# Optimization experiments

Measured on AMD Instinct MI355X. Metric: run time of the kernel, lower is better.

## Reference

```python
import jax, jax.numpy as jnp
import numpy as np

N, B, I = 64, 32, 1
EMBED, ACT, DETER, STOCH, HIDDEN = 1536, 16, 2048, 512, 1024
EPS = 1e-5


def _ln(x, g, b):
    m = jnp.mean(x, -1, keepdims=True)
    v = jnp.mean((x - m) ** 2, -1, keepdims=True)
    return (x - m) / jnp.sqrt(v + EPS) * g + b


def setup_inputs() -> dict:
    key = jax.random.key(0)
    ks = jax.random.split(key, 24)
    s = 0.02
    d = {
        "embed": jax.random.normal(ks[0], (N, B, EMBED), jnp.float32),
        "action": jax.random.normal(ks[1], (N, B, ACT), jnp.float32),
        "reset": jnp.zeros((N, B), jnp.bool_),
        "h0": jnp.zeros((B * I, DETER), jnp.float32),
        "z0": jnp.zeros((B * I, STOCH), jnp.float32),
        "noises": jax.random.normal(ks[2], (N, B, I, STOCH), jnp.float32),
        # params
        "W_z": jax.random.normal(ks[3], (HIDDEN, STOCH)) * s,
        "b_z": jnp.zeros((HIDDEN,)),
        "W_a": jax.random.normal(ks[4], (HIDDEN, ACT)) * s,
        "ln_in_g": jnp.ones((HIDDEN,)), "ln_in_b": jnp.zeros((HIDDEN,)),
        "gru_Wih": jax.random.normal(ks[5], (3 * DETER, HIDDEN)) * s,
        "gru_Whh": jax.random.normal(ks[6], (3 * DETER, DETER)) * s,
        "gru_bih": jnp.zeros((3 * DETER,)), "gru_bhh": jnp.zeros((3 * DETER,)),
        "W_ph": jax.random.normal(ks[7], (HIDDEN, DETER)) * s,
        "b_ph": jnp.zeros((HIDDEN,)),
        "W_pe": jax.random.normal(ks[8], (HIDDEN, EMBED)) * s,
        "ln_post_g": jnp.ones((HIDDEN,)), "ln_post_b": jnp.zeros((HIDDEN,)),
        "W_post": jax.random.normal(ks[9], (2 * STOCH, HIDDEN)) * s,
        "b_post": jnp.zeros((2 * STOCH,)),
        "W_prh": jax.random.normal(ks[10], (HIDDEN, DETER)) * s,
        "b_prh": jnp.zeros((HIDDEN,)),
        "ln_pr_g": jnp.ones((HIDDEN,)), "ln_pr_b": jnp.zeros((HIDDEN,)),
        "W_pr": jax.random.normal(ks[11], (2 * STOCH, HIDDEN)) * s,
        "b_pr": jnp.zeros((2 * STOCH,)),
    }
    return d


def _core(embed, action, reset, h0, z0, noises,
          W_z, b_z, W_a, ln_in_g, ln_in_b,
          gru_Wih, gru_Whh, gru_bih, gru_bhh,
          W_ph, b_ph, W_pe, ln_post_g, ln_post_b, W_post, b_post,
          W_prh, b_prh, ln_pr_g, ln_pr_b, W_pr, b_pr):
    n, b = embed.shape[:2]
    # expand to (n, b*I, .) ; I == 1
    embeds = embed.reshape(n, b * I, -1)
    actions = action.reshape(n, b * I, -1)
    masks = (~reset).astype(jnp.float32).reshape(n, b * I, 1)
    noise = noises.reshape(n, b * I, -1)

    def step(carry, xs):
        h, z = carry
        e_t, a_t, m_t, n_t = xs
        h = h * m_t
        z = z * m_t
        x = z @ W_z.T + b_z + a_t @ W_a.T
        za = jax.nn.elu(_ln(x, ln_in_g, ln_in_b))
        # torch GRUCell
        gi = za @ gru_Wih.T + gru_bih
        gh = h @ gru_Whh.T + gru_bhh
        gi_r, gi_u, gi_n = jnp.split(gi, 3, -1)
        gh_r, gh_u, gh_n = jnp.split(gh, 3, -1)
        r = jax.nn.sigmoid(gi_r + gh_r)
        u = jax.nn.sigmoid(gi_u + gh_u)
        cand = jnp.tanh(gi_n + r * gh_n)
        h_new = (1.0 - u) * cand + u * h
        x = h_new @ W_ph.T + b_ph + e_t @ W_pe.T
        post_in = jax.nn.elu(_ln(x, ln_post_g, ln_post_b))
        post = post_in @ W_post.T + b_post
        mean, std_raw = jnp.split(post, 2, -1)
        std = jax.nn.softplus(std_raw) + 0.1
        sample = mean + std * n_t
        return (h_new, sample), (post, h_new, sample)

    (h_last, z_last), (posts, states_h, samples) = jax.lax.scan(
        step, (h0, z0), (embeds, actions, masks, noise))

    # batch prior over all h
    x = states_h @ W_prh.T + b_prh
    x = jax.nn.elu(_ln(x, ln_pr_g, ln_pr_b))
    priors = x @ W_pr.T + b_pr
    features = jnp.concatenate([states_h, samples], -1)

    rs = lambda t: t.reshape(n, b, I, -1)
    return rs(priors), rs(posts), rs(samples), rs(features), h_last, z_last


def reference(embed, action, reset, h0, z0, noises,
              W_z, b_z, W_a, ln_in_g, ln_in_b,
              gru_Wih, gru_Whh, gru_bih, gru_bhh,
              W_ph, b_ph, W_pe, ln_post_g, ln_post_b, W_post, b_post,
              W_prh, b_prh, ln_pr_g, ln_pr_b, W_pr, b_pr):
    return _core(embed, action, reset, h0, z0, noises,
                 W_z, b_z, W_a, ln_in_g, ln_in_b,
                 gru_Wih, gru_Whh, gru_bih, gru_bhh,
                 W_ph, b_ph, W_pe, ln_post_g, ln_post_b, W_post, b_post,
                 W_prh, b_prh, ln_pr_g, ln_pr_b, W_pr, b_pr)
```

## Files before the change

### kernel.cpp

```cpp
#include <hip/hip_runtime.h>
#include <hip/hip_bf16.h>
#include <stdint.h>

#define NSTEP 64
#define BATCH 32
#define EMBED_D 1536
#define ACT_D 16
#define DETER 2048
#define STOCH 512
#define HIDDEN 1024
#define FEAT 2560
#define NBLK 256

typedef __attribute__((ext_vector_type(8))) short bf16x8;
typedef __attribute__((ext_vector_type(4))) float f32x4;

#define MFMA16 __builtin_amdgcn_mfma_f32_16x16x32_bf16
#define AGENT __HIP_MEMORY_SCOPE_AGENT

__device__ __forceinline__ float eluf(float x) { return x > 0.f ? x : expf(x) - 1.f; }
__device__ __forceinline__ float sigf(float x) { return 1.f / (1.f + expf(-x)); }
__device__ __forceinline__ unsigned short f2bf(float f) {
    __hip_bfloat16 h = __float2bfloat16(f);
    return __builtin_bit_cast(unsigned short, h);
}
__device__ __forceinline__ float bf2f(unsigned short u) {
    unsigned v = ((unsigned)u) << 16;
    return __builtin_bit_cast(float, v);
}

__device__ __forceinline__ void stc_u32(unsigned* p, unsigned v) {
    __hip_atomic_store(p, v, __ATOMIC_RELAXED, AGENT);
}
__device__ __forceinline__ void stc_u64(unsigned long long* p, unsigned long long v) {
    __hip_atomic_store(p, v, __ATOMIC_RELAXED, AGENT);
}
__device__ __forceinline__ unsigned long long ldc_u64(const unsigned long long* p) {
    return __hip_atomic_load(p, __ATOMIC_RELAXED, AGENT);
}
__device__ __forceinline__ float ldc_f32(const float* p) {
    return __hip_atomic_load(p, __ATOMIC_RELAXED, AGENT);
}
__device__ __forceinline__ int ldc_i32(const int* p) {
    return __hip_atomic_load(p, __ATOMIC_RELAXED, AGENT);
}
__device__ __forceinline__ void stc_i32(int* p, int v) {
    __hip_atomic_store(p, v, __ATOMIC_RELAXED, AGENT);
}
__device__ __forceinline__ bf16x8 ldc_bf8(const unsigned short* p) {
    union { unsigned long long q[2]; bf16x8 v; } u;
    u.q[0] = ldc_u64((const unsigned long long*)p);
    u.q[1] = ldc_u64((const unsigned long long*)(p + 4));
    return u.v;
}
__device__ __forceinline__ ushort4 ldc_us4(const unsigned short* p) {
    unsigned long long q = ldc_u64((const unsigned long long*)p);
    return __builtin_bit_cast(ushort4, q);
}

__device__ __forceinline__ void gbar3(int* flags, int* release, int epoch) {
    asm volatile("s_waitcnt vmcnt(0)" ::: "memory");
    __syncthreads();
    if (blockIdx.x == 0) {
        int tid = threadIdx.x;
        if (tid >= 1 && tid < NBLK) {
            while (ldc_i32(&flags[tid * 32]) < epoch) __builtin_amdgcn_s_sleep(4);
        }
        asm volatile("" ::: "memory");
        __syncthreads();
        if (tid < 32) stc_i32(&release[tid * 32], epoch);
    } else {
        if (threadIdx.x == 0) {
            stc_i32(&flags[blockIdx.x * 32], epoch);
            int* rel = &release[(blockIdx.x & 31) * 32];
            while (ldc_i32(rel) < epoch) __builtin_amdgcn_s_sleep(4);
        }
        asm volatile("" ::: "memory");
        __syncthreads();
    }
}

__global__ __launch_bounds__(256) void k_cvt_all(
    const float* __restrict__ s0, unsigned short* __restrict__ d0,
    const float* __restrict__ s1, unsigned short* __restrict__ d1,
    const float* __restrict__ s2, unsigned short* __restrict__ d2,
    const float* __restrict__ s3, unsigned short* __restrict__ d3,
    const float* __restrict__ s4, unsigned short* __restrict__ d4)
{
    long long e = ((long long)blockIdx.x * 256 + threadIdx.x) * 4;
    const float* src; unsigned short* dst; long long off;
    if (e < 524288)        { src = s0; dst = d0; off = e; }
    else if (e < 6815744)  { src = s1; dst = d1; off = e - 524288; }
    else if (e < 19398656) { src = s2; dst = d2; off = e - 6815744; }
    else if (e < 21495808) { src = s3; dst = d3; off = e - 19398656; }
    else if (e < 22544384) { src = s4; dst = d4; off = e - 21495808; }
    else return;
    float4 v = *reinterpret_cast<const float4*>(src + off);
    ushort4 o;
    o.x = f2bf(v.x); o.y = f2bf(v.y); o.z = f2bf(v.z); o.w = f2bf(v.w);
    *reinterpret_cast<ushort4*>(dst + off) = o;
}

__global__ __launch_bounds__(256) void k_setup(
    const float* __restrict__ h0, const float* __restrict__ z0,
    const uint8_t* __restrict__ reset0,
    float* __restrict__ h0m, unsigned short* __restrict__ h16m0,
    unsigned short* __restrict__ z16m, int* __restrict__ flags)
{
    int gid = blockIdx.x * 256 + threadIdx.x;
    int idx = gid * 4;
    if (idx < BATCH * DETER) {
        int b = idx >> 11;
        float m = reset0[b] ? 0.f : 1.f;
        float4 v = *reinterpret_cast<const float4*>(h0 + idx);
        v.x *= m; v.y *= m; v.z *= m; v.w *= m;
        *reinterpret_cast<float4*>(h0m + idx) = v;
        ushort4 o;
        o.x = f2bf(v.x); o.y = f2bf(v.y); o.z = f2bf(v.z); o.w = f2bf(v.w);
        *reinterpret_cast<ushort4*>(h16m0 + idx) = o;
    } else if (idx < BATCH * DETER + BATCH * STOCH) {
        int zi = idx - BATCH * DETER;
        int b = zi >> 9;
        float m = reset0[b] ? 0.f : 1.f;
        float4 v = *reinterpret_cast<const float4*>(z0 + zi);
        ushort4 o;
        o.x = f2bf(v.x * m); o.y = f2bf(v.y * m); o.z = f2bf(v.z * m); o.w = f2bf(v.w * m);
        *reinterpret_cast<ushort4*>(z16m + zi) = o;
    }
    if (gid < 9216) flags[gid] = 0;
}

__global__ __launch_bounds__(256) void k_preA(
    const float* __restrict__ action, const float* __restrict__ Wa,
    const float* __restrict__ bz, float* __restrict__ preA)
{
    __shared__ float al[16];
    int r = blockIdx.x, t = threadIdx.x;
    if (t < 16) al[t] = action[r * 16 + t];
    __syncthreads();
#pragma unroll
    for (int c = 0; c < 4; ++c) {
        int j = t + c * 256;
        const float* wr = Wa + j * 16;
        float s = bz[j];
#pragma unroll
        for (int k = 0; k < 16; ++k) s += al[k] * wr[k];
        preA[(size_t)r * 1024 + j] = s;
    }
}

__global__ __launch_bounds__(256) void gemm_mfma(
    const float* __restrict__ A, int lda,
    const float* __restrict__ B, int ldb,
    const float* __restrict__ bias,
    float* __restrict__ C, int ldc, int K)
{
    __shared__ unsigned short Alds[64 * 72];
    __shared__ unsigned short Blds[64 * 72];
    int t = threadIdx.x;
    int nb = blockIdx.x, mb = blockIdx.y;
    int w = t >> 6, l = t & 63, l15 = l & 15, kg = l >> 4;
    f32x4 acc[4] = {{0,0,0,0},{0,0,0,0},{0,0,0,0},{0,0,0,0}};
    int srow = t >> 2, skq = (t & 3) * 16;
    const float* Asrc = A + (size_t)(mb * 64 + srow) * lda + skq;
    const float* Bsrc = B + (size_t)(nb * 64 + srow) * ldb + skq;
    unsigned short* Adst = &Alds[srow * 72 + skq];
    unsigned short* Bdst = &Blds[srow * 72 + skq];
    for (int kt = 0; kt < K; kt += 64) {
        __syncthreads();
#pragma unroll
        for (int c = 0; c < 16; c += 4) {
            float4 va = *reinterpret_cast<const float4*>(Asrc + kt + c);
            float4 vb = *reinterpret_cast<const float4*>(Bsrc + kt + c);
            ushort4 oa, ob;
            oa.x = f2bf(va.x); oa.y = f2bf(va.y); oa.z = f2bf(va.z); oa.w = f2bf(va.w);
            ob.x = f2bf(vb.x); ob.y = f2bf(vb.y); ob.z = f2bf(vb.z); ob.w = f2bf(vb.w);
            *reinterpret_cast<ushort4*>(Adst + c) = oa;
            *reinterpret_cast<ushort4*>(Bdst + c) = ob;
        }
        __syncthreads();
#pragma unroll
        for (int ks = 0; ks < 2; ks++) {
            bf16x8 a = *reinterpret_cast<const bf16x8*>(&Alds[(w * 16 + l15) * 72 + ks * 32 + kg * 8]);
#pragma unroll
            for (int nt = 0; nt < 4; nt++) {
                bf16x8 b = *reinterpret_cast<const bf16x8*>(&Blds[(nt * 16 + l15) * 72 + ks * 32 + kg * 8]);
                acc[nt] = MFMA16(a, b, acc[nt], 0, 0, 0);
            }
        }
    }
#pragma unroll
    for (int nt = 0; nt < 4; nt++) {
        int n = nb * 64 + nt * 16 + l15;
        float bv = bias[n];
#pragma unroll
        for (int i = 0; i < 4; i++) {
            C[(size_t)(mb * 64 + w * 16 + kg * 4 + i) * ldc + n] = acc[nt][i] + bv;
        }
    }
}

__global__ __launch_bounds__(256) void ln_elu_rows(
    float* __restrict__ X, const float* __restrict__ g, const float* __restrict__ bb)
{
    __shared__ float sbuf[256], qbuf[256];
    int r = blockIdx.x, t = threadIdx.x;
    float* row = X + (size_t)r * HIDDEN;
    float4 v = reinterpret_cast<const float4*>(row)[t];
    sbuf[t] = (v.x + v.y) + (v.z + v.w);
    qbuf[t] = (v.x * v.x + v.y * v.y) + (v.z * v.z + v.w * v.w);
    __syncthreads();
    for (int off = 128; off > 0; off >>= 1) {
        if (t < off) { sbuf[t] += sbuf[t + off]; qbuf[t] += qbuf[t + off]; }
        __syncthreads();
    }
    float mean = sbuf[0] / HIDDEN;
    float var = qbuf[0] / HIDDEN - mean * mean;
    float rstd = rsqrtf(var + 1e-5f);
    float4 gg = reinterpret_cast<const float4*>(g)[t];
    float4 bv = reinterpret_cast<const float4*>(bb)[t];
    float4 o;
    o.x = eluf((v.x - mean) * rstd * gg.x + bv.x);
    o.y = eluf((v.y - mean) * rstd * gg.y + bv.y);
    o.z = eluf((v.z - mean) * rstd * gg.z + bv.z);
    o.w = eluf((v.w - mean) * rstd * gg.w + bv.w);
    reinterpret_cast<float4*>(row)[t] = o;
}

__global__ __launch_bounds__(256) void k_copy_last(
    const float* __restrict__ feat63, const float* __restrict__ samp63,
    float* __restrict__ hlast, float* __restrict__ zlast)
{
    int i = blockIdx.x * 256 + threadIdx.x;
    if (i < BATCH * DETER) {
        int b = i / DETER, k = i % DETER;
        hlast[i] = feat63[(size_t)b * FEAT + k];
    }
    if (i < BATCH * STOCH) zlast[i] = samp63[i];
}

struct ScanArgs {
    const unsigned short *Wz16, *Wih16, *Whh16, *Wph16, *Wpo16;
    const float *bih, *bhh, *b_post;
    const float *ln_in_g, *ln_in_b, *ln_post_g, *ln_post_b;
    const float *h0m;
    const uint8_t *reset;
    const float *noises;
    float *postsPreA;
    float *priorsPreE;
    float *samples;
    float *feats;
    unsigned short *z16m, *x1b, *x2b, *h16u, *h16m0, *h16m1;
    float *x1parts, *x2parts;
    int *flags, *release;
};

__device__ __forceinline__ void ln_stats(const float* __restrict__ parts, float* stat, int tid) {
    if (tid < 32) {
        float s = 0.f, q = 0.f;
        for (int i = 0; i < 64; ++i) {
            union { unsigned long long u; float f[2]; } c;
            c.u = ldc_u64((const unsigned long long*)(parts + (size_t)(i * 32 + tid) * 2));
            s += c.f[0]; q += c.f[1];
        }
        float mean = s * (1.f / 1024.f);
        float var = q * (1.f / 1024.f) - mean * mean;
        stat[tid] = mean;
        stat[32 + tid] = rsqrtf(var + 1e-5f);
    }
}

__device__ __forceinline__ void ln_fill(unsigned short* Asm, const unsigned short* __restrict__ src,
                                        const float* __restrict__ g, const float* __restrict__ bb,
                                        const float* stat, int tid) {
    int row = tid & 31, kb = (tid >> 5) * 128;
    float mean = stat[row], rstd = stat[32 + row];
#pragma unroll 4
    for (int c = 0; c < 16; ++c) {
        int k = kb + c * 8;
        ushort4 u0 = ldc_us4(src + (size_t)row * 1024 + k);
        ushort4 u1 = ldc_us4(src + (size_t)row * 1024 + k + 4);
        float4 g0 = *reinterpret_cast<const float4*>(g + k);
        float4 g1 = *reinterpret_cast<const float4*>(g + k + 4);
        float4 b0 = *reinterpret_cast<const float4*>(bb + k);
        float4 b1 = *reinterpret_cast<const float4*>(bb + k + 4);
        ushort4 o0, o1;
        o0.x = f2bf(eluf((bf2f(u0.x) - mean) * rstd * g0.x + b0.x));
        o0.y = f2bf(eluf((bf2f(u0.y) - mean) * rstd * g0.y + b0.y));
        o0.z = f2bf(eluf((bf2f(u0.z) - mean) * rstd * g0.z + b0.z));
        o0.w = f2bf(eluf((bf2f(u0.w) - mean) * rstd * g0.w + b0.w));
        o1.x = f2bf(eluf((bf2f(u1.x) - mean) * rstd * g1.x + b1.x));
        o1.y = f2bf(eluf((bf2f(u1.y) - mean) * rstd * g1.y + b1.y));
        o1.z = f2bf(eluf((bf2f(u1.z) - mean) * rstd * g1.z + b1.z));
        o1.w = f2bf(eluf((bf2f(u1.w) - mean) * rstd * g1.w + b1.w));
        *reinterpret_cast<ushort4*>(Asm + row * 1032 + k) = o0;
        *reinterpret_cast<ushort4*>(Asm + row * 1032 + k + 4) = o1;
    }
}

__global__ __launch_bounds__(256, 1) void k_scan(ScanArgs a) {
    __shared__ char smem[90112];
    unsigned short* Asm = (unsigned short*)smem;
    float* cbuf = (float*)(smem + 66048);
    float* stat = (float*)(smem + 66048 + 8192);

    const int bid = blockIdx.x;
    const int tid = threadIdx.x;
    const int w = tid >> 6, l = tid & 63, l15 = l & 15, kg = l >> 4;
    int epoch = 0;

    for (int t = 0; t < NSTEP; ++t) {
        const float* preA_t = a.postsPreA + (size_t)t * 32768;
        const float* preE_t = a.priorsPreE + (size_t)t * 32768;
        float* posts_t = a.postsPreA + (size_t)t * 32768;
        float* samples_t = a.samples + (size_t)t * 16384;
        float* feats_t = a.feats + (size_t)t * 81920;
        const float* featsPrev = a.feats + (size_t)(t - 1) * 81920;
        const unsigned short* h16cur = (t & 1) ? a.h16m1 : a.h16m0;
        unsigned short* h16nxt = (t & 1) ? a.h16m0 : a.h16m1;

        if (bid < 64) {
            int j0 = bid * 16;
            const unsigned short* A0 = a.z16m + l15 * 512 + w * 128 + kg * 8;
            const unsigned short* A1 = A0 + 16 * 512;
            const unsigned short* Bp = a.Wz16 + (size_t)(j0 + l15) * 512 + w * 128 + kg * 8;
            f32x4 c0 = {0,0,0,0}, c1 = {0,0,0,0};
#pragma unroll
            for (int ks = 0; ks < 4; ++ks) {
                bf16x8 b = *reinterpret_cast<const bf16x8*>(Bp + ks * 32);
                c0 = MFMA16(ldc_bf8(A0 + ks * 32), b, c0, 0, 0, 0);
                c1 = MFMA16(ldc_bf8(A1 + ks * 32), b, c1, 0, 0, 0);
            }
#pragma unroll
            for (int i = 0; i < 4; ++i) {
                cbuf[w * 512 + (kg * 4 + i) * 16 + l15] = c0[i];
                cbuf[w * 512 + (16 + kg * 4 + i) * 16 + l15] = c1[i];
            }
            __syncthreads();
            int r = tid >> 3, c2 = (tid & 7) * 2;
            int base = r * 16 + c2;
            float v0 = cbuf[base] + cbuf[512 + base] + cbuf[1024 + base] + cbuf[1536 + base]
                     + preA_t[r * 1024 + j0 + c2];
            float v1 = cbuf[base + 1] + cbuf[512 + base + 1] + cbuf[1024 + base + 1] + cbuf[1536 + base + 1]
                     + preA_t[r * 1024 + j0 + c2 + 1];
            unsigned short u0 = f2bf(v0), u1 = f2bf(v1);
            stc_u32((unsigned*)(a.x1b + (size_t)r * 1024 + j0 + c2),
                    (unsigned)u0 | ((unsigned)u1 << 16));
            float w0 = bf2f(u0), w1 = bf2f(u1);
            float s = w0 + w1, q = w0 * w0 + w1 * w1;
            s += __shfl_xor(s, 1); q += __shfl_xor(q, 1);
            s += __shfl_xor(s, 2); q += __shfl_xor(q, 2);
            s += __shfl_xor(s, 4); q += __shfl_xor(q, 4);
            if ((tid & 7) == 0) {
                union { float f[2]; unsigned long long u; } pu;
                pu.f[0] = s; pu.f[1] = q;
                stc_u64((unsigned long long*)(a.x1parts + ((size_t)bid * 32 + r) * 2), pu.u);
            }
        }
        epoch++; gbar3(a.flags, a.release, epoch);

        if (bid < 128) {
            int j0 = bid * 16;
            ln_stats(a.x1parts, stat, tid);
            __syncthreads();
            ln_fill(Asm, a.x1b, a.ln_in_g, a.ln_in_b, stat, tid);
            __syncthreads();
            bool isI = (w < 2);
            int mt = w & 1;
            f32x4 cr = {0,0,0,0}, cu = {0,0,0,0}, cn = {0,0,0,0};
            if (isI) {
                const unsigned short* ap = Asm + (mt * 16 + l15) * 1032 + kg * 8;
                const unsigned short* br = a.Wih16 + (size_t)(j0 + l15) * 1024 + kg * 8;
                const unsigned short* bu = br + (size_t)2048 * 1024;
                const unsigned short* bn = bu + (size_t)2048 * 1024;
#pragma unroll 8
                for (int ks = 0; ks < 32; ++ks) {
                    bf16x8 av = *reinterpret_cast<const bf16x8*>(ap + ks * 32);
                    cr = MFMA16(av, *reinterpret_cast<const bf16x8*>(br + ks * 32), cr, 0, 0, 0);
                    cu = MFMA16(av, *reinterpret_cast<const bf16x8*>(bu + ks * 32), cu, 0, 0, 0);
                    cn = MFMA16(av, *reinterpret_cast<const bf16x8*>(bn + ks * 32), cn, 0, 0, 0);
                }
            } else {
                const unsigned short* ap = h16cur + (size_t)(mt * 16 + l15) * 2048 + kg * 8;
                const unsigned short* br = a.Whh16 + (size_t)(j0 + l15) * 2048 + kg * 8;
                const unsigned short* bu = br + (size_t)2048 * 2048;
                const unsigned short* bn = bu + (size_t)2048 * 2048;
#pragma unroll 8
                for (int ks = 0; ks < 64; ++ks) {
                    bf16x8 av = ldc_bf8(ap + ks * 32);
                    cr = MFMA16(av, *reinterpret_cast<const bf16x8*>(br + ks * 32), cr, 0, 0, 0);
                    cu = MFMA16(av, *reinterpret_cast<const bf16x8*>(bu + ks * 32), cu, 0, 0, 0);
                    cn = MFMA16(av, *reinterpret_cast<const bf16x8*>(bn + ks * 32), cn, 0, 0, 0);
                }
#pragma unroll
                for (int i = 0; i < 4; ++i) {
                    cbuf[((mt * 3 + 0) * 16 + kg * 4 + i) * 16 + l15] = cr[i];
                    cbuf[((mt * 3 + 1) * 16 + kg * 4 + i) * 16 + l15] = cu[i];
                    cbuf[((mt * 3 + 2) * 16 + kg * 4 + i) * 16 + l15] = cn[i];
                }
            }
            __syncthreads();
            if (isI) {
                int j = j0 + l15;
                float bihr = a.bih[j], bihu = a.bih[j + 2048], bihn = a.bih[j + 4096];
                float bhhr = a.bhh[j], bhhu = a.bhh[j + 2048], bhhn = a.bhh[j + 4096];
#pragma unroll
                for (int i = 0; i < 4; ++i) {
                    int b = mt * 16 + kg * 4 + i;
                    float gr = cr[i] + bihr, gu = cu[i] + bihu, gn = cn[i] + bihn;
                    float hr = cbuf[((mt * 3 + 0) * 16 + kg * 4 + i) * 16 + l15] + bhhr;
                    float hu = cbuf[((mt * 3 + 1) * 16 + kg * 4 + i) * 16 + l15] + bhhu;
                    float hn = cbuf[((mt * 3 + 2) * 16 + kg * 4 + i) * 16 + l15] + bhhn;
                    float r = sigf(gr + hr), u = sigf(gu + hu);
                    float cand = tanhf(gn + r * hn);
                    float m = a.reset[t * 32 + b] ? 0.f : 1.f;
                    float hpv = (t == 0) ? a.h0m[b * 2048 + j]
                                         : ldc_f32(featsPrev + (size_t)b * 2560 + j);
                    float hnew = (1.f - u) * cand + u * (m * hpv);
                    cbuf[1536 + b * 16 + l15] = hnew;
                }
            }
            __syncthreads();
            {
                int b = tid >> 3, c2 = (tid & 7) * 2;
                float h0v = cbuf[1536 + b * 16 + c2], h1v = cbuf[1536 + b * 16 + c2 + 1];
                int j = j0 + c2;
                union { float f[2]; unsigned long long u; } fu;
                fu.f[0] = h0v; fu.f[1] = h1v;
                stc_u64((unsigned long long*)(feats_t + (size_t)b * 2560 + j), fu.u);
                unsigned short g0 = f2bf(h0v), g1 = f2bf(h1v);
                stc_u32((unsigned*)(a.h16u + (size_t)b * 2048 + j),
                        (unsigned)g0 | ((unsigned)g1 << 16));
                float mn = (t < 63) ? (a.reset[(t + 1) * 32 + b] ? 0.f : 1.f) : 1.f;
                unsigned short n0 = f2bf(h0v * mn), n1 = f2bf(h1v * mn);
                stc_u32((unsigned*)(h16nxt + (size_t)b * 2048 + j),
                        (unsigned)n0 | ((unsigned)n1 << 16));
            }
        }
        epoch++; gbar3(a.flags, a.release, epoch);

        if (bid < 64) {
            int j0 = bid * 16;
            const unsigned short* A0 = a.h16u + l15 * 2048 + w * 512 + kg * 8;
            const unsigned short* A1 = A0 + 16 * 2048;
            const unsigned short* Bp = a.Wph16 + (size_t)(j0 + l15) * 2048 + w * 512 + kg * 8;
            f32x4 c0 = {0,0,0,0}, c1 = {0,0,0,0};
#pragma unroll 8
            for (int ks = 0; ks < 16; ++ks) {
                bf16x8 b = *reinterpret_cast<const bf16x8*>(Bp + ks * 32);
                c0 = MFMA16(ldc_bf8(A0 + ks * 32), b, c0, 0, 0, 0);
                c1 = MFMA16(ldc_bf8(A1 + ks * 32), b, c1, 0, 0, 0);
            }
#pragma unroll
            for (int i = 0; i < 4; ++i) {
                cbuf[w * 512 + (kg * 4 + i) * 16 + l15] = c0[i];
                cbuf[w * 512 + (16 + kg * 4 + i) * 16 + l15] = c1[i];
            }
            __syncthreads();
            int r = tid >> 3, c2 = (tid & 7) * 2;
            int base = r * 16 + c2;
            float v0 = cbuf[base] + cbuf[512 + base] + cbuf[1024 + base] + cbuf[1536 + base]
                     + preE_t[r * 1024 + j0 + c2];
            float v1 = cbuf[base + 1] + cbuf[512 + base + 1] + cbuf[1024 + base + 1] + cbuf[1536 + base + 1]
                     + preE_t[r * 1024 + j0 + c2 + 1];
            unsigned short u0 = f2bf(v0), u1 = f2bf(v1);
            stc_u32((unsigned*)(a.x2b + (size_t)r * 1024 + j0 + c2),
                    (unsigned)u0 | ((unsigned)u1 << 16));
            float w0 = bf2f(u0), w1 = bf2f(u1);
            float s = w0 + w1, q = w0 * w0 + w1 * w1;
            s += __shfl_xor(s, 1); q += __shfl_xor(q, 1);
            s += __shfl_xor(s, 2); q += __shfl_xor(q, 2);
            s += __shfl_xor(s, 4); q += __shfl_xor(q, 4);
            if ((tid & 7) == 0) {
                union { float f[2]; unsigned long long u; } pu;
                pu.f[0] = s; pu.f[1] = q;
                stc_u64((unsigned long long*)(a.x2parts + ((size_t)bid * 32 + r) * 2), pu.u);
            }
        }
        epoch++; gbar3(a.flags, a.release, epoch);

        if (bid < 32) {
            int j0 = bid * 16;
            ln_stats(a.x2parts, stat, tid);
            __syncthreads();
            ln_fill(Asm, a.x2b, a.ln_post_g, a.ln_post_b, stat, tid);
            __syncthreads();
            int tile = w >> 1, mt = w & 1;
            const unsigned short* ap = Asm + (mt * 16 + l15) * 1032 + kg * 8;
            int n = (tile == 0) ? (j0 + l15) : (512 + j0 + l15);
            const unsigned short* Bp = a.Wpo16 + (size_t)n * 1024 + kg * 8;
            f32x4 c = {0,0,0,0};
#pragma unroll 8
            for (int ks = 0; ks < 32; ++ks) {
                c = MFMA16(*reinterpret_cast<const bf16x8*>(ap + ks * 32),
                           *reinterpret_cast<const bf16x8*>(Bp + ks * 32), c, 0, 0, 0);
            }
#pragma unroll
            for (int i = 0; i < 4; ++i)
                cbuf[(tile * 2 + mt) * 256 + (kg * 4 + i) * 16 + l15] = c[i];
            __syncthreads();
            int b = tid >> 3, c2 = (tid & 7) * 2;
            int j = j0 + c2;
            int ib = (b >> 4) * 256 + (b & 15) * 16;
            float pm0 = cbuf[ib + c2] + a.b_post[j];
            float pm1 = cbuf[ib + c2 + 1] + a.b_post[j + 1];
            float ps0 = cbuf[512 + ib + c2] + a.b_post[512 + j];
            float ps1 = cbuf[512 + ib + c2 + 1] + a.b_post[512 + j + 1];
            posts_t[(size_t)b * 1024 + j] = pm0;
            posts_t[(size_t)b * 1024 + j + 1] = pm1;
            posts_t[(size_t)b * 1024 + 512 + j] = ps0;
            posts_t[(size_t)b * 1024 + 512 + j + 1] = ps1;
            float sp0 = fmaxf(ps0, 0.f) + log1pf(expf(-fabsf(ps0)));
            float sp1 = fmaxf(ps1, 0.f) + log1pf(expf(-fabsf(ps1)));
            float n0v = a.noises[(size_t)t * 16384 + b * 512 + j];
            float n1v = a.noises[(size_t)t * 16384 + b * 512 + j + 1];
            float smp0 = pm0 + (sp0 + 0.1f) * n0v;
            float smp1 = pm1 + (sp1 + 0.1f) * n1v;
            samples_t[(size_t)b * 512 + j] = smp0;
            samples_t[(size_t)b * 512 + j + 1] = smp1;
            feats_t[(size_t)b * 2560 + 2048 + j] = smp0;
            feats_t[(size_t)b * 2560 + 2048 + j + 1] = smp1;
            float mn = (t < 63) ? (a.reset[(t + 1) * 32 + b] ? 0.f : 1.f) : 1.f;
            unsigned short z0_ = f2bf(smp0 * mn), z1_ = f2bf(smp1 * mn);
            stc_u32((unsigned*)(a.z16m + (size_t)b * 512 + j),
                    (unsigned)z0_ | ((unsigned)z1_ << 16));
        }
        epoch++; gbar3(a.flags, a.release, epoch);
    }
}

#define WS_WZ16   ((size_t)0)
#define WS_WIH16  ((size_t)1048576)
#define WS_WHH16  ((size_t)13631488)
#define WS_WPH16  ((size_t)38797312)
#define WS_WPO16  ((size_t)42991616)
#define WS_Z16M   ((size_t)45088768)
#define WS_H16M0  ((size_t)45121536)
#define WS_H16M1  ((size_t)45252608)
#define WS_H16U   ((size_t)45383680)
#define WS_H0M    ((size_t)45514752)
#define WS_X1B    ((size_t)45776896)
#define WS_X2B    ((size_t)45842432)
#define WS_X1P    ((size_t)45907968)
#define WS_X2P    ((size_t)45924352)
#define WS_FLAGS  ((size_t)45940736)
#define WS_REL    ((size_t)45973504)
#define WS_PRX    WS_WIH16

extern "C" void kernel_launch(void* const* d_in, const int* in_sizes, int n_in,
                              void* d_out, int out_size, void* d_ws, size_t ws_size,
                              hipStream_t stream)
{
    (void)in_sizes; (void)n_in; (void)out_size; (void)ws_size;
    const float*   embed  = (const float*)d_in[0];
    const float*   action = (const float*)d_in[1];
    const uint8_t* reset  = (const uint8_t*)d_in[2];
    const float*   h0     = (const float*)d_in[3];
    const float*   z0     = (const float*)d_in[4];
    const float*   noises = (const float*)d_in[5];
    const float*   W_z    = (const float*)d_in[6];
    const float*   b_z    = (const float*)d_in[7];
    const float*   W_a    = (const float*)d_in[8];
    const float*   ln_in_g = (const float*)d_in[9];
    const float*   ln_in_b = (const float*)d_in[10];
    const float*   Wih    = (const float*)d_in[11];
    const float*   Whh    = (const float*)d_in[12];
    const float*   bih    = (const float*)d_in[13];
    const float*   bhh    = (const float*)d_in[14];
    const float*   W_ph   = (const float*)d_in[15];
    const float*   b_ph   = (const float*)d_in[16];
    const float*   W_pe   = (const float*)d_in[17];
    const float*   ln_post_g = (const float*)d_in[18];
    const float*   ln_post_b = (const float*)d_in[19];
    const float*   W_post = (const float*)d_in[20];
    const float*   b_post = (const float*)d_in[21];
    const float*   W_prh  = (const float*)d_in[22];
    const float*   b_prh  = (const float*)d_in[23];
    const float*   ln_pr_g = (const float*)d_in[24];
    const float*   ln_pr_b = (const float*)d_in[25];
    const float*   W_pr   = (const float*)d_in[26];
    const float*   b_pr   = (const float*)d_in[27];

    float* out     = (float*)d_out;
    float* priors  = out;
    float* posts   = out + 2097152;
    float* samples = out + 4194304;
    float* feats   = out + 5242880;
    float* hlast   = out + 10485760;
    float* zlast   = out + 10551296;

    char* ws = (char*)d_ws;
    unsigned short* Wz16  = (unsigned short*)(ws + WS_WZ16);
    unsigned short* Wih16 = (unsigned short*)(ws + WS_WIH16);
    unsigned short* Whh16 = (unsigned short*)(ws + WS_WHH16);
    unsigned short* Wph16 = (unsigned short*)(ws + WS_WPH16);
    unsigned short* Wpo16 = (unsigned short*)(ws + WS_WPO16);
    unsigned short* z16m  = (unsigned short*)(ws + WS_Z16M);
    unsigned short* h16m0 = (unsigned short*)(ws + WS_H16M0);
    unsigned short* h16m1 = (unsigned short*)(ws + WS_H16M1);
    unsigned short* h16u  = (unsigned short*)(ws + WS_H16U);
    float*          h0m   = (float*)(ws + WS_H0M);
    unsigned short* x1b   = (unsigned short*)(ws + WS_X1B);
    unsigned short* x2b   = (unsigned short*)(ws + WS_X2B);
    float*          x1p   = (float*)(ws + WS_X1P);
    float*          x2p   = (float*)(ws + WS_X2P);
    int*            flags = (int*)(ws + WS_FLAGS);
    int*            release = (int*)(ws + WS_REL);
    float*          prx   = (float*)(ws + WS_PRX);

    dim3 blk(256);

    k_cvt_all<<<dim3(22016), blk, 0, stream>>>(W_z, Wz16, Wih, Wih16, Whh, Whh16,
                                               W_ph, Wph16, W_post, Wpo16);
    k_setup<<<dim3(80), blk, 0, stream>>>(h0, z0, reset, h0m, h16m0, z16m, flags);

    k_preA<<<dim3(2048), blk, 0, stream>>>(action, W_a, b_z, posts);
    gemm_mfma<<<dim3(16, 32), blk, 0, stream>>>(embed, EMBED_D, W_pe, EMBED_D, b_ph,
                                                priors, HIDDEN, EMBED_D);

    ScanArgs sa;
    sa.Wz16 = Wz16; sa.Wih16 = Wih16; sa.Whh16 = Whh16; sa.Wph16 = Wph16; sa.Wpo16 = Wpo16;
    sa.bih = bih; sa.bhh = bhh; sa.b_post = b_post;
    sa.ln_in_g = ln_in_g; sa.ln_in_b = ln_in_b; sa.ln_post_g = ln_post_g; sa.ln_post_b = ln_post_b;
    sa.h0m = h0m; sa.reset = reset; sa.noises = noises;
    sa.postsPreA = posts; sa.priorsPreE = priors; sa.samples = samples; sa.feats = feats;
    sa.z16m = z16m; sa.x1b = x1b; sa.x2b = x2b; sa.h16u = h16u;
    sa.h16m0 = h16m0; sa.h16m1 = h16m1;
    sa.x1parts = x1p; sa.x2parts = x2p;
    sa.flags = flags; sa.release = release;
    k_scan<<<dim3(NBLK), blk, 0, stream>>>(sa);

    gemm_mfma<<<dim3(16, 32), blk, 0, stream>>>(feats, FEAT, W_prh, DETER, b_prh,
                                                prx, HIDDEN, DETER);
    ln_elu_rows<<<dim3(2048), blk, 0, stream>>>(prx, ln_pr_g, ln_pr_b);
    gemm_mfma<<<dim3(16, 32), blk, 0, stream>>>(prx, HIDDEN, W_pr, HIDDEN, b_pr,
                                                priors, HIDDEN, HIDDEN);

    k_copy_last<<<dim3(256), blk, 0, stream>>>(
        feats + (size_t)(NSTEP - 1) * BATCH * FEAT,
        samples + (size_t)(NSTEP - 1) * BATCH * STOCH,
        hlast, zlast);
}
```

Measured before the change: 4.676 ms.

## Double scan block size and split GRU K-dimension across eight waves

The persistent scan kernel now launches with 512 threads per block. The GRU stage splits each input-side and hidden-side matmul's K dimension in half across twice as many waves, then reduces the partial sums through shared memory before the gate math. The aim is to shorten the per-step critical path, which is dominated by streaming the GRU weights. Other stages leave the extra waves idle behind tid<256 guards. This adds shared-memory reduction traffic and raises per-block register pressure.

```diff
diff --git a/kernel.cpp b/kernel.cpp
--- a/kernel.cpp
+++ b/kernel.cpp
@@ -246,10 +246,7 @@
     const float *h0m;
     const uint8_t *reset;
     const float *noises;
-    float *postsPreA;
-    float *priorsPreE;
-    float *samples;
-    float *feats;
+    float *postsPreA, *priorsPreE, *samples, *feats;
     unsigned short *z16m, *x1b, *x2b, *h16u, *h16m0, *h16m1;
     float *x1parts, *x2parts;
     int *flags, *release;
@@ -298,11 +295,13 @@
     }
 }
 
-__global__ __launch_bounds__(256, 1) void k_scan(ScanArgs a) {
-    __shared__ char smem[90112];
+__global__ __launch_bounds__(512, 1) void k_scan(ScanArgs a) {
+    __shared__ char smem[93184];
     unsigned short* Asm = (unsigned short*)smem;
-    float* cbuf = (float*)(smem + 66048);
-    float* stat = (float*)(smem + 66048 + 8192);
+    float* cbuf  = (float*)(smem + 66048);
+    float* stat  = (float*)(smem + 66048 + 8192);
+    float* stat2 = (float*)(smem + 90624);
+    float* hbuf  = (float*)(smem + 91136);
 
     const int bid = blockIdx.x;
     const int tid = threadIdx.x;
@@ -321,109 +320,112 @@
 
         if (bid < 64) {
             int j0 = bid * 16;
-            const unsigned short* A0 = a.z16m + l15 * 512 + w * 128 + kg * 8;
-            const unsigned short* A1 = A0 + 16 * 512;
-            const unsigned short* Bp = a.Wz16 + (size_t)(j0 + l15) * 512 + w * 128 + kg * 8;
-            f32x4 c0 = {0,0,0,0}, c1 = {0,0,0,0};
-#pragma unroll
-            for (int ks = 0; ks < 4; ++ks) {
-                bf16x8 b = *reinterpret_cast<const bf16x8*>(Bp + ks * 32);
-                c0 = MFMA16(ldc_bf8(A0 + ks * 32), b, c0, 0, 0, 0);
-                c1 = MFMA16(ldc_bf8(A1 + ks * 32), b, c1, 0, 0, 0);
-            }
-#pragma unroll
-            for (int i = 0; i < 4; ++i) {
-                cbuf[w * 512 + (kg * 4 + i) * 16 + l15] = c0[i];
-                cbuf[w * 512 + (16 + kg * 4 + i) * 16 + l15] = c1[i];
-            }
-            __syncthreads();
-            int r = tid >> 3, c2 = (tid & 7) * 2;
-            int base = r * 16 + c2;
-            float v0 = cbuf[base] + cbuf[512 + base] + cbuf[1024 + base] + cbuf[1536 + base]
-                     + preA_t[r * 1024 + j0 + c2];
-            float v1 = cbuf[base + 1] + cbuf[512 + base + 1] + cbuf[1024 + base + 1] + cbuf[1536 + base + 1]
-                     + preA_t[r * 1024 + j0 + c2 + 1];
-            unsigned short u0 = f2bf(v0), u1 = f2bf(v1);
-            stc_u32((unsigned*)(a.x1b + (size_t)r * 1024 + j0 + c2),
-                    (unsigned)u0 | ((unsigned)u1 << 16));
-            float w0 = bf2f(u0), w1 = bf2f(u1);
-            float s = w0 + w1, q = w0 * w0 + w1 * w1;
-            s += __shfl_xor(s, 1); q += __shfl_xor(q, 1);
-            s += __shfl_xor(s, 2); q += __shfl_xor(q, 2);
-            s += __shfl_xor(s, 4); q += __shfl_xor(q, 4);
-            if ((tid & 7) == 0) {
-                union { float f[2]; unsigned long long u; } pu;
-                pu.f[0] = s; pu.f[1] = q;
-                stc_u64((unsigned long long*)(a.x1parts + ((size_t)bid * 32 + r) * 2), pu.u);
+            if (tid < 256) {
+                const unsigned short* A0 = a.z16m + l15 * 512 + w * 128 + kg * 8;
+                const unsigned short* A1 = A0 + 16 * 512;
+                const unsigned short* Bp = a.Wz16 + (size_t)(j0 + l15) * 512 + w * 128 + kg * 8;
+                f32x4 c0 = {0,0,0,0}, c1 = {0,0,0,0};
+#pragma unroll
+                for (int ks = 0; ks < 4; ++ks) {
+                    bf16x8 b = *reinterpret_cast<const bf16x8*>(Bp + ks * 32);
+                    c0 = MFMA16(ldc_bf8(A0 + ks * 32), b, c0, 0, 0, 0);
+                    c1 = MFMA16(ldc_bf8(A1 + ks * 32), b, c1, 0, 0, 0);
+                }
+#pragma unroll
+                for (int i = 0; i < 4; ++i) {
+                    cbuf[w * 512 + (kg * 4 + i) * 16 + l15] = c0[i];
+                    cbuf[w * 512 + (16 + kg * 4 + i) * 16 + l15] = c1[i];
+                }
+            }
+            __syncthreads();
+            if (tid < 256) {
+                int r = tid >> 3, c2 = (tid & 7) * 2;
+                int base = r * 16 + c2;
+                float v0 = cbuf[base] + cbuf[512 + base] + cbuf[1024 + base] + cbuf[1536 + base]
+                         + preA_t[r * 1024 + j0 + c2];
+                float v1 = cbuf[base + 1] + cbuf[512 + base + 1] + cbuf[1024 + base + 1] + cbuf[1536 + base + 1]
+                         + preA_t[r * 1024 + j0 + c2 + 1];
+                unsigned short u0 = f2bf(v0), u1 = f2bf(v1);
+                stc_u32((unsigned*)(a.x1b + (size_t)r * 1024 + j0 + c2),
+                        (unsigned)u0 | ((unsigned)u1 << 16));
+                float w0 = bf2f(u0), w1 = bf2f(u1);
+                float s = w0 + w1, q = w0 * w0 + w1 * w1;
+                s += __shfl_xor(s, 1); q += __shfl_xor(q, 1);
+                s += __shfl_xor(s, 2); q += __shfl_xor(q, 2);
+                s += __shfl_xor(s, 4); q += __shfl_xor(q, 4);
+                if ((tid & 7) == 0) {
+                    union { float f[2]; unsigned long long u; } pu;
+                    pu.f[0] = s; pu.f[1] = q;
+                    stc_u64((unsigned long long*)(a.x1parts + ((size_t)bid * 32 + r) * 2), pu.u);
+                }
             }
         }
         epoch++; gbar3(a.flags, a.release, epoch);
 
         if (bid < 128) {
             int j0 = bid * 16;
-            ln_stats(a.x1parts, stat, tid);
-            __syncthreads();
-            ln_fill(Asm, a.x1b, a.ln_in_g, a.ln_in_b, stat, tid);
-            __syncthreads();
-            bool isI = (w < 2);
-            int mt = w & 1;
+            ln_stats(a.x1parts, stat2, tid);
+            __syncthreads();
+            if (tid < 256) ln_fill(Asm, a.x1b, a.ln_in_g, a.ln_in_b, stat2, tid);
+            __syncthreads();
             f32x4 cr = {0,0,0,0}, cu = {0,0,0,0}, cn = {0,0,0,0};
-            if (isI) {
-                const unsigned short* ap = Asm + (mt * 16 + l15) * 1032 + kg * 8;
-                const unsigned short* br = a.Wih16 + (size_t)(j0 + l15) * 1024 + kg * 8;
+            if (w < 4) {
+                int rowgrp = w & 1, kh = w >> 1;
+                const unsigned short* ap = Asm + (rowgrp * 16 + l15) * 1032 + kh * 512 + kg * 8;
+                const unsigned short* br = a.Wih16 + (size_t)(j0 + l15) * 1024 + kh * 512 + kg * 8;
                 const unsigned short* bu = br + (size_t)2048 * 1024;
                 const unsigned short* bn = bu + (size_t)2048 * 1024;
-#pragma unroll 8
-                for (int ks = 0; ks < 32; ++ks) {
+#pragma unroll 4
+                for (int ks = 0; ks < 16; ++ks) {
                     bf16x8 av = *reinterpret_cast<const bf16x8*>(ap + ks * 32);
                     cr = MFMA16(av, *reinterpret_cast<const bf16x8*>(br + ks * 32), cr, 0, 0, 0);
                     cu = MFMA16(av, *reinterpret_cast<const bf16x8*>(bu + ks * 32), cu, 0, 0, 0);
                     cn = MFMA16(av, *reinterpret_cast<const bf16x8*>(bn + ks * 32), cn, 0, 0, 0);
                 }
             } else {
-                const unsigned short* ap = h16cur + (size_t)(mt * 16 + l15) * 2048 + kg * 8;
-                const unsigned short* br = a.Whh16 + (size_t)(j0 + l15) * 2048 + kg * 8;
+                int idx = w - 4, rowgrp = idx & 1, kh = idx >> 1;
+                const unsigned short* hp = h16cur + (size_t)(rowgrp * 16 + l15) * 2048 + kh * 1024 + kg * 8;
+                const unsigned short* br = a.Whh16 + (size_t)(j0 + l15) * 2048 + kh * 1024 + kg * 8;
                 const unsigned short* bu = br + (size_t)2048 * 2048;
                 const unsigned short* bn = bu + (size_t)2048 * 2048;
-#pragma unroll 8
-                for (int ks = 0; ks < 64; ++ks) {
-                    bf16x8 av = ldc_bf8(ap + ks * 32);
+#pragma unroll 4
+                for (int ks = 0; ks < 32; ++ks) {
+                    bf16x8 av = ldc_bf8(hp + ks * 32);
                     cr = MFMA16(av, *reinterpret_cast<const bf16x8*>(br + ks * 32), cr, 0, 0, 0);
                     cu = MFMA16(av, *reinterpret_cast<const bf16x8*>(bu + ks * 32), cu, 0, 0, 0);
                     cn = MFMA16(av, *reinterpret_cast<const bf16x8*>(bn + ks * 32), cn, 0, 0, 0);
                 }
-#pragma unroll
-                for (int i = 0; i < 4; ++i) {
-                    cbuf[((mt * 3 + 0) * 16 + kg * 4 + i) * 16 + l15] = cr[i];
-                    cbuf[((mt * 3 + 1) * 16 + kg * 4 + i) * 16 + l15] = cu[i];
-                    cbuf[((mt * 3 + 2) * 16 + kg * 4 + i) * 16 + l15] = cn[i];
-                }
-            }
-            __syncthreads();
-            if (isI) {
-                int j = j0 + l15;
-                float bihr = a.bih[j], bihu = a.bih[j + 2048], bihn = a.bih[j + 4096];
-                float bhhr = a.bhh[j], bhhu = a.bhh[j + 2048], bhhn = a.bhh[j + 4096];
-#pragma unroll
-                for (int i = 0; i < 4; ++i) {
-                    int b = mt * 16 + kg * 4 + i;
-                    float gr = cr[i] + bihr, gu = cu[i] + bihu, gn = cn[i] + bihn;
-                    float hr = cbuf[((mt * 3 + 0) * 16 + kg * 4 + i) * 16 + l15] + bhhr;
-                    float hu = cbuf[((mt * 3 + 1) * 16 + kg * 4 + i) * 16 + l15] + bhhu;
-                    float hn = cbuf[((mt * 3 + 2) * 16 + kg * 4 + i) * 16 + l15] + bhhn;
-                    float r = sigf(gr + hr), u = sigf(gu + hu);
-                    float cand = tanhf(gn + r * hn);
-                    float m = a.reset[t * 32 + b] ? 0.f : 1.f;
-                    float hpv = (t == 0) ? a.h0m[b * 2048 + j]
-                                         : ldc_f32(featsPrev + (size_t)b * 2560 + j);
-                    float hnew = (1.f - u) * cand + u * (m * hpv);
-                    cbuf[1536 + b * 16 + l15] = hnew;
-                }
+            }
+#pragma unroll
+            for (int i = 0; i < 4; ++i) {
+                int o = (kg * 4 + i) * 16 + l15;
+                cbuf[w * 768 + 0 * 256 + o] = cr[i];
+                cbuf[w * 768 + 1 * 256 + o] = cu[i];
+                cbuf[w * 768 + 2 * 256 + o] = cn[i];
             }
             __syncthreads();
             {
+                int row = tid >> 4, col = tid & 15;
+                int rowgrp = row >> 4, rr = row & 15;
+                int o = rr * 16 + col;
+                int j = j0 + col;
+                float gr = cbuf[rowgrp * 768 + 0 * 256 + o] + cbuf[(2 + rowgrp) * 768 + 0 * 256 + o] + a.bih[j];
+                float gu = cbuf[rowgrp * 768 + 1 * 256 + o] + cbuf[(2 + rowgrp) * 768 + 1 * 256 + o] + a.bih[j + 2048];
+                float gn = cbuf[rowgrp * 768 + 2 * 256 + o] + cbuf[(2 + rowgrp) * 768 + 2 * 256 + o] + a.bih[j + 4096];
+                float hr = cbuf[(4 + rowgrp) * 768 + 0 * 256 + o] + cbuf[(6 + rowgrp) * 768 + 0 * 256 + o] + a.bhh[j];
+                float hu = cbuf[(4 + rowgrp) * 768 + 1 * 256 + o] + cbuf[(6 + rowgrp) * 768 + 1 * 256 + o] + a.bhh[j + 2048];
+                float hn = cbuf[(4 + rowgrp) * 768 + 2 * 256 + o] + cbuf[(6 + rowgrp) * 768 + 2 * 256 + o] + a.bhh[j + 4096];
+                float r_ = sigf(gr + hr), u_ = sigf(gu + hu);
+                float cand = tanhf(gn + r_ * hn);
+                float m = a.reset[t * 32 + row] ? 0.f : 1.f;
+                float hpv = (t == 0) ? a.h0m[(size_t)row * 2048 + j]
+                                     : ldc_f32(featsPrev + (size_t)row * 2560 + j);
+                hbuf[row * 16 + col] = (1.f - u_) * cand + u_ * (m * hpv);
+            }
+            __syncthreads();
+            if (tid < 256) {
                 int b = tid >> 3, c2 = (tid & 7) * 2;
-                float h0v = cbuf[1536 + b * 16 + c2], h1v = cbuf[1536 + b * 16 + c2 + 1];
+                float h0v = hbuf[b * 16 + c2], h1v = hbuf[b * 16 + c2 + 1];
                 int j = j0 + c2;
                 union { float f[2]; unsigned long long u; } fu;
                 fu.f[0] = h0v; fu.f[1] = h1v;
@@ -441,40 +443,44 @@
 
         if (bid < 64) {
             int j0 = bid * 16;
-            const unsigned short* A0 = a.h16u + l15 * 2048 + w * 512 + kg * 8;
-            const unsigned short* A1 = A0 + 16 * 2048;
-            const unsigned short* Bp = a.Wph16 + (size_t)(j0 + l15) * 2048 + w * 512 + kg * 8;
-            f32x4 c0 = {0,0,0,0}, c1 = {0,0,0,0};
+            if (tid < 256) {
+                const unsigned short* A0 = a.h16u + l15 * 2048 + w * 512 + kg * 8;
+                const unsigned short* A1 = A0 + 16 * 2048;
+                const unsigned short* Bp = a.Wph16 + (size_t)(j0 + l15) * 2048 + w * 512 + kg * 8;
+                f32x4 c0 = {0,0,0,0}, c1 = {0,0,0,0};
 #pragma unroll 8
-            for (int ks = 0; ks < 16; ++ks) {
-                bf16x8 b = *reinterpret_cast<const bf16x8*>(Bp + ks * 32);
-                c0 = MFMA16(ldc_bf8(A0 + ks * 32), b, c0, 0, 0, 0);
-                c1 = MFMA16(ldc_bf8(A1 + ks * 32), b, c1, 0, 0, 0);
-            }
-#pragma unroll
-            for (int i = 0; i < 4; ++i) {
-                cbuf[w * 512 + (kg * 4 + i) * 16 + l15] = c0[i];
-                cbuf[w * 512 + (16 + kg * 4 + i) * 16 + l15] = c1[i];
-            }
-            __syncthreads();
-            int r = tid >> 3, c2 = (tid & 7) * 2;
-            int base = r * 16 + c2;
-            float v0 = cbuf[base] + cbuf[512 + base] + cbuf[1024 + base] + cbuf[1536 + base]
-                     + preE_t[r * 1024 + j0 + c2];
-            float v1 = cbuf[base + 1] + cbuf[512 + base + 1] + cbuf[1024 + base + 1] + cbuf[1536 + base + 1]
-                     + preE_t[r * 1024 + j0 + c2 + 1];
-            unsigned short u0 = f2bf(v0), u1 = f2bf(v1);
-            stc_u32((unsigned*)(a.x2b + (size_t)r * 1024 + j0 + c2),
-                    (unsigned)u0 | ((unsigned)u1 << 16));
-            float w0 = bf2f(u0), w1 = bf2f(u1);
-            float s = w0 + w1, q = w0 * w0 + w1 * w1;
-            s += __shfl_xor(s, 1); q += __shfl_xor(q, 1);
-            s += __shfl_xor(s, 2); q += __shfl_xor(q, 2);
-            s += __shfl_xor(s, 4); q += __shfl_xor(q, 4);
-            if ((tid & 7) == 0) {
-                union { float f[2]; unsigned long long u; } pu;
-                pu.f[0] = s; pu.f[1] = q;
-                stc_u64((unsigned long long*)(a.x2parts + ((size_t)bid * 32 + r) * 2), pu.u);
+                for (int ks = 0; ks < 16; ++ks) {
+                    bf16x8 b = *reinterpret_cast<const bf16x8*>(Bp + ks * 32);
+                    c0 = MFMA16(ldc_bf8(A0 + ks * 32), b, c0, 0, 0, 0);
+                    c1 = MFMA16(ldc_bf8(A1 + ks * 32), b, c1, 0, 0, 0);
+                }
+#pragma unroll
+                for (int i = 0; i < 4; ++i) {
+                    cbuf[w * 512 + (kg * 4 + i) * 16 + l15] = c0[i];
+                    cbuf[w * 512 + (16 + kg * 4 + i) * 16 + l15] = c1[i];
+                }
+            }
+            __syncthreads();
+            if (tid < 256) {
+                int r = tid >> 3, c2 = (tid & 7) * 2;
+                int base = r * 16 + c2;
+                float v0 = cbuf[base] + cbuf[512 + base] + cbuf[1024 + base] + cbuf[1536 + base]
+                         + preE_t[r * 1024 + j0 + c2];
+                float v1 = cbuf[base + 1] + cbuf[512 + base + 1] + cbuf[1024 + base + 1] + cbuf[1536 + base + 1]
+                         + preE_t[r * 1024 + j0 + c2 + 1];
+                unsigned short u0 = f2bf(v0), u1 = f2bf(v1);
+                stc_u32((unsigned*)(a.x2b + (size_t)r * 1024 + j0 + c2),
+                        (unsigned)u0 | ((unsigned)u1 << 16));
+                float w0 = bf2f(u0), w1 = bf2f(u1);
+                float s = w0 + w1, q = w0 * w0 + w1 * w1;
+                s += __shfl_xor(s, 1); q += __shfl_xor(q, 1);
+                s += __shfl_xor(s, 2); q += __shfl_xor(q, 2);
+                s += __shfl_xor(s, 4); q += __shfl_xor(q, 4);
+                if ((tid & 7) == 0) {
+                    union { float f[2]; unsigned long long u; } pu;
+                    pu.f[0] = s; pu.f[1] = q;
+                    stc_u64((unsigned long long*)(a.x2parts + ((size_t)bid * 32 + r) * 2), pu.u);
+                }
             }
         }
         epoch++; gbar3(a.flags, a.release, epoch);
@@ -483,47 +489,51 @@
             int j0 = bid * 16;
             ln_stats(a.x2parts, stat, tid);
             __syncthreads();
-            ln_fill(Asm, a.x2b, a.ln_post_g, a.ln_post_b, stat, tid);
-            __syncthreads();
-            int tile = w >> 1, mt = w & 1;
-            const unsigned short* ap = Asm + (mt * 16 + l15) * 1032 + kg * 8;
-            int n = (tile == 0) ? (j0 + l15) : (512 + j0 + l15);
-            const unsigned short* Bp = a.Wpo16 + (size_t)n * 1024 + kg * 8;
-            f32x4 c = {0,0,0,0};
+            if (tid < 256) ln_fill(Asm, a.x2b, a.ln_post_g, a.ln_post_b, stat, tid);
+            __syncthreads();
+            if (tid < 256) {
+                int tile = w >> 1, mt = w & 1;
+                const unsigned short* ap = Asm + (mt * 16 + l15) * 1032 + kg * 8;
+                int n = (tile == 0) ? (j0 + l15) : (512 + j0 + l15);
+                const unsigned short* Bp = a.Wpo16 + (size_t)n * 1024 + kg * 8;
+                f32x4 c = {0,0,0,0};
 #pragma unroll 8
-            for (int ks = 0; ks < 32; ++ks) {
-                c = MFMA16(*reinterpret_cast<const bf16x8*>(ap + ks * 32),
-                           *reinterpret_cast<const bf16x8*>(Bp + ks * 32), c, 0, 0, 0);
-            }
-#pragma unroll
-            for (int i = 0; i < 4; ++i)
-                cbuf[(tile * 2 + mt) * 256 + (kg * 4 + i) * 16 + l15] = c[i];
-            __syncthreads();
-            int b = tid >> 3, c2 = (tid & 7) * 2;
-            int j = j0 + c2;
-            int ib = (b >> 4) * 256 + (b & 15) * 16;
-            float pm0 = cbuf[ib + c2] + a.b_post[j];
-            float pm1 = cbuf[ib + c2 + 1] + a.b_post[j + 1];
-            float ps0 = cbuf[512 + ib + c2] + a.b_post[512 + j];
-            float ps1 = cbuf[512 + ib + c2 + 1] + a.b_post[512 + j + 1];
-            posts_t[(size_t)b * 1024 + j] = pm0;
-            posts_t[(size_t)b * 1024 + j + 1] = pm1;
-            posts_t[(size_t)b * 1024 + 512 + j] = ps0;
-            posts_t[(size_t)b * 1024 + 512 + j + 1] = ps1;
-            float sp0 = fmaxf(ps0, 0.f) + log1pf(expf(-fabsf(ps0)));
-            float sp1 = fmaxf(ps1, 0.f) + log1pf(expf(-fabsf(ps1)));
-            float n0v = a.noises[(size_t)t * 16384 + b * 512 + j];
-            float n1v = a.noises[(size_t)t * 16384 + b * 512 + j + 1];
-            float smp0 = pm0 + (sp0 + 0.1f) * n0v;
-            float smp1 = pm1 + (sp1 + 0.1f) * n1v;
-            samples_t[(size_t)b * 512 + j] = smp0;
-            samples_t[(size_t)b * 512 + j + 1] = smp1;
-            feats_t[(size_t)b * 2560 + 2048 + j] = smp0;
-            feats_t[(size_t)b * 2560 + 2048 + j + 1] = smp1;
-            float mn = (t < 63) ? (a.reset[(t + 1) * 32 + b] ? 0.f : 1.f) : 1.f;
-            unsigned short z0_ = f2bf(smp0 * mn), z1_ = f2bf(smp1 * mn);
-            stc_u32((unsigned*)(a.z16m + (size_t)b * 512 + j),
-                    (unsigned)z0_ | ((unsigned)z1_ << 16));
+                for (int ks = 0; ks < 32; ++ks) {
+                    c = MFMA16(*reinterpret_cast<const bf16x8*>(ap + ks * 32),
+                               *reinterpret_cast<const bf16x8*>(Bp + ks * 32), c, 0, 0, 0);
+                }
+#pragma unroll
+                for (int i = 0; i < 4; ++i)
+                    cbuf[(tile * 2 + mt) * 256 + (kg * 4 + i) * 16 + l15] = c[i];
+            }
+            __syncthreads();
+            if (tid < 256) {
+                int b = tid >> 3, c2 = (tid & 7) * 2;
+                int j = j0 + c2;
+                int ib = (b >> 4) * 256 + (b & 15) * 16;
+                float pm0 = cbuf[ib + c2] + a.b_post[j];
+                float pm1 = cbuf[ib + c2 + 1] + a.b_post[j + 1];
+                float ps0 = cbuf[512 + ib + c2] + a.b_post[512 + j];
+                float ps1 = cbuf[512 + ib + c2 + 1] + a.b_post[512 + j + 1];
+                posts_t[(size_t)b * 1024 + j] = pm0;
+                posts_t[(size_t)b * 1024 + j + 1] = pm1;
+                posts_t[(size_t)b * 1024 + 512 + j] = ps0;
+                posts_t[(size_t)b * 1024 + 512 + j + 1] = ps1;
+                float sp0 = fmaxf(ps0, 0.f) + log1pf(expf(-fabsf(ps0)));
+                float sp1 = fmaxf(ps1, 0.f) + log1pf(expf(-fabsf(ps1)));
+                float n0v = a.noises[(size_t)t * 16384 + b * 512 + j];
+                float n1v = a.noises[(size_t)t * 16384 + b * 512 + j + 1];
+                float smp0 = pm0 + (sp0 + 0.1f) * n0v;
+                float smp1 = pm1 + (sp1 + 0.1f) * n1v;
+                samples_t[(size_t)b * 512 + j] = smp0;
+                samples_t[(size_t)b * 512 + j + 1] = smp1;
+                feats_t[(size_t)b * 2560 + 2048 + j] = smp0;
+                feats_t[(size_t)b * 2560 + 2048 + j + 1] = smp1;
+                float mn = (t < 63) ? (a.reset[(t + 1) * 32 + b] ? 0.f : 1.f) : 1.f;
+                unsigned short z0_ = f2bf(smp0 * mn), z1_ = f2bf(smp1 * mn);
+                stc_u32((unsigned*)(a.z16m + (size_t)b * 512 + j),
+                        (unsigned)z0_ | ((unsigned)z1_ << 16));
+            }
         }
         epoch++; gbar3(a.flags, a.release, epoch);
     }
@@ -628,7 +638,8 @@
     sa.h16m0 = h16m0; sa.h16m1 = h16m1;
     sa.x1parts = x1p; sa.x2parts = x2p;
     sa.flags = flags; sa.release = release;
-    k_scan<<<dim3(NBLK), blk, 0, stream>>>(sa);
+
+    k_scan<<<dim3(NBLK), dim3(512), 0, stream>>>(sa);
 
     gemm_mfma<<<dim3(16, 32), blk, 0, stream>>>(feats, FEAT, W_prh, DETER, b_prh,
                                                 prx, HIDDEN, DETER);
```

Measured after the change: 4.510 ms. 3.5% less time.
